# Performance work log

Hardware: AMD Instinct MI355X
Metric: run time of the kernel (lower is better)

The kernel has to match this reference:

```python
import jax, jax.numpy as jnp
import numpy as np

N = 70
NT = 2485
M_DIM = 2000
SQ2 = float(np.sqrt(2.0))
SQH = float(np.sqrt(0.5))
_r, _c = np.tril_indices(N)
ROWS = jnp.asarray(_r)
COLS = jnp.asarray(_c)


def smat(x):
    # svec^{-1}: lower-tri fill (row-major) then symmetrize with sqrt(2) off-diag scaling
    v = jnp.reshape(x, (-1,))
    L = jnp.zeros((N, N), v.dtype).at[ROWS, COLS].set(v)
    return SQH * (L + L.T) - (SQ2 - 1.0) * L * jnp.eye(N, dtype=v.dtype)


def svec(X):
    Y = SQ2 * X - (SQ2 - 1.0) * X * jnp.eye(N, dtype=X.dtype)
    return Y[ROWS, COLS].reshape(NT, 1)


def skmult(G, K, Amat):
    # vectorized version of the per-column loop: for each column a of Amat,
    # 0.5 * svec(K smat(a) G^T + G smat(a) K^T)
    S = jax.vmap(smat, in_axes=1)(Amat)                      # [L, N, N]
    T = jnp.einsum('ij,ljk,hk->lih', K, S, G) + jnp.einsum('ij,ljk,hk->lih', G, S, K)
    return jax.vmap(svec)(0.5 * T)[:, :, 0].T                # [NT, L]


def Hp_op(U, P, Pinv):
    return 0.5 * (P @ U @ Pinv + Pinv.T @ U.T @ P.T)


def _steplen(d, Rinv, gcur):
    lam0 = jnp.linalg.eigvalsh(Rinv.T @ smat(d) @ Rinv)[0]   # smallest eigenvalue
    s = jnp.where(lam0 < 0, -1.0 / lam0, 20.0)
    return jnp.minimum(0.5, gcur * s)


def setup_inputs() -> dict:
    key = jax.random.key(0)
    ks = jax.random.split(key, 6)
    R1 = jax.random.normal(ks[0], (N, N), jnp.float32)
    X0 = R1 @ R1.T + N * jnp.eye(N, dtype=jnp.float32)
    R2 = jax.random.normal(ks[1], (N, N), jnp.float32)
    Z0 = R2 @ R2.T + N * jnp.eye(N, dtype=jnp.float32)
    x = svec(X0)
    z = svec(Z0)
    A = jax.random.normal(ks[2], (M_DIM, NT), jnp.float32) / np.float32(np.sqrt(NT))
    y = jax.random.normal(ks[3], (M_DIM, 1), jnp.float32)
    b = A @ x + 0.1 * jax.random.normal(ks[4], (M_DIM, 1), jnp.float32)
    c = z + A.T @ y + 0.1 * jax.random.normal(ks[5], (NT, 1), jnp.float32)
    normc = jnp.full((1, 1), 3.7, jnp.float32)
    return {'x': x, 'y': y, 'z': z, 'A': A, 'b': b, 'c': c, 'normc': normc}


def reference(x, y, z, A, b, c, normc):
    tol = 1e-6
    X = smat(x)
    Z = smat(z)
    Q = jnp.linalg.cholesky(X).T        # upper factor: X = Q^T Q
    P = jnp.linalg.cholesky(Z).T
    Qinv = jnp.linalg.inv(Q)
    Pinv = jnp.linalg.inv(P)
    Zinv = jnp.linalg.inv(Z)
    rp = b - A @ x
    Rd = c - z - A.T @ y
    mu = (x[:, 0] @ z[:, 0]) / 70.0
    # predictor
    Rc = -svec(Hp_op(X @ Z, P, Pinv))
    Mmat = A @ skmult(X, Zinv, A.T)
    Minv = jnp.linalg.inv(Mmat)
    h = rp + A @ (skmult(X, Zinv, Rd) - skmult(Pinv, Pinv, Rc))
    dy = Minv @ h
    dz = Rd - A.T @ dy
    dx = -x - skmult(X, Zinv, dz)
    alpha = _steplen(dx, Qinv, 0.9)
    beta = _steplen(dz, Pinv, 0.9)
    minab = jnp.minimum(alpha, beta)
    e = jnp.where((mu > tol) & (minab >= jnp.sqrt(1.0 / 3.0)),
                  jnp.maximum(1.0, 3.0 * minab * minab), 1.0)
    dot_new = (x + alpha * dx)[:, 0] @ (z + beta * dz)[:, 0]
    frac = dot_new / (x[:, 0] @ z[:, 0])
    frac_safe = jnp.where(dot_new < 0, 1.0, frac)
    sigma = jnp.where(dot_new < 0, 0.8, jnp.minimum(1.0, frac_safe ** e))
    # corrector
    Rc2 = svec(sigma * mu * jnp.eye(N, dtype=x.dtype)
               - Hp_op(X @ Z, P, Pinv)
               - Hp_op(smat(dx) @ smat(dz), P, Pinv))
    h2 = rp + A @ (skmult(X, Zinv, Rd) - skmult(Pinv, Pinv, Rc2))
    dy2 = Minv @ h2
    dz2 = Rd - A.T @ dy2
    dx2 = skmult(Pinv, Pinv, Rc2) - skmult(X, Zinv, dz2)
    g2 = 0.9 + 0.09 * minab
    alpha2 = _steplen(dx2, Qinv, g2)
    beta2 = _steplen(dz2, Pinv, g2)
    x_new = x + alpha2 * dx2
    y_new = y + beta2 * dy2
    z_new = z + beta2 * dz2
    y1 = y_new * normc
    return (x_new, y_new, z_new, y1)
```

## Files before the change

### kernel.cpp

```cpp
#include <hip/hip_runtime.h>
#include <math.h>

#define SQHf 0.70710678118654752440f

struct Pairs16 { int4 q[16]; };

__device__ __forceinline__ void d_t2ij(int t, int& i, int& j) {
    float f = sqrtf(8.0f * (float)t + 1.0f);
    int r = (int)((f - 1.0f) * 0.5f);
    while (((r + 1) * (r + 2)) / 2 <= t) ++r;
    while ((r * (r + 1)) / 2 > t) --r;
    i = r;
    j = t - (r * (r + 1)) / 2;
}

__global__ void k_smat2(const float* __restrict__ v1, float* __restrict__ M1,
                        const float* __restrict__ v2, float* __restrict__ M2) {
    int idx = blockIdx.x * 256 + threadIdx.x;
    if (idx >= 9800) return;
    int which = idx / 4900;
    int e = idx - which * 4900;
    const float* v = which ? v2 : v1;
    float* M = which ? M2 : M1;
    int i = e / 70, j = e % 70;
    int hi = i > j ? i : j, lo = i > j ? j : i;
    float val = v[(hi * (hi + 1)) / 2 + lo];
    M[e] = (i == j) ? val : val * SQHf;
}

__global__ __launch_bounds__(256) void k_chol2(const float* __restrict__ A0, float* __restrict__ R0,
                                               const float* __restrict__ A1, float* __restrict__ R1) {
    const float* A = blockIdx.x ? A1 : A0;
    float* R = blockIdx.x ? R1 : R0;
    __shared__ float S[70][71];
    for (int e = threadIdx.x; e < 4900; e += 256) S[e / 70][e % 70] = A[e];
    __syncthreads();
    for (int k = 0; k < 70; ++k) {
        if (threadIdx.x == 0) S[k][k] = sqrtf(S[k][k]);
        __syncthreads();
        float d = S[k][k];
        for (int i = k + 1 + threadIdx.x; i < 70; i += 256) S[i][k] /= d;
        __syncthreads();
        for (int e = threadIdx.x; e < 4900; e += 256) {
            int i = e / 70, j = e % 70;
            if (j > k && i >= j) S[i][j] -= S[i][k] * S[j][k];
        }
        __syncthreads();
    }
    for (int e = threadIdx.x; e < 4900; e += 256) {
        int i = e / 70, j = e % 70;
        R[e] = (i <= j) ? S[j][i] : 0.0f;
    }
}

__global__ __launch_bounds__(256) void k_trinv2(const float* __restrict__ R0, float* __restrict__ O0,
                                                const float* __restrict__ R1, float* __restrict__ O1) {
    const float* R = blockIdx.x ? R1 : R0;
    float* O = blockIdx.x ? O1 : O0;
    __shared__ float S[70][71];
    __shared__ float V[70][71];
    for (int e = threadIdx.x; e < 4900; e += 256) S[e / 70][e % 70] = R[e];
    __syncthreads();
    int j = threadIdx.x;
    if (j < 70) {
        for (int i = j; i >= 0; --i) {
            float s = (i == j) ? 1.0f : 0.0f;
            for (int k = i + 1; k <= j; ++k) s -= S[i][k] * V[j][k];
            V[j][i] = s / S[i][i];
        }
    }
    __syncthreads();
    for (int e = threadIdx.x; e < 4900; e += 256) {
        int i = e / 70, jj = e % 70;
        O[e] = (i <= jj) ? V[jj][i] : 0.0f;
    }
}

__global__ __launch_bounds__(256) void k_mm70(const float* __restrict__ A, int tA,
                                              const float* __restrict__ B, int tB,
                                              float* __restrict__ C) {
    __shared__ float As[70][71], Bs[70][71];
    for (int e = threadIdx.x; e < 4900; e += 256) {
        int i = e / 70, j = e % 70;
        As[i][j] = tA ? A[j * 70 + i] : A[e];
        Bs[i][j] = tB ? B[j * 70 + i] : B[e];
    }
    __syncthreads();
    for (int e = threadIdx.x; e < 4900; e += 256) {
        int i = e / 70, j = e % 70;
        float s = 0.0f;
        for (int k = 0; k < 70; ++k) s += As[i][k] * Bs[k][j];
        C[e] = s;
    }
}

__global__ __launch_bounds__(256) void k_gemv_rowA(const float* __restrict__ A, long lda, int Kdim,
                                                   const float* __restrict__ v, const float* __restrict__ add,
                                                   float sgn, float* __restrict__ out) {
    int row = blockIdx.x;
    const float* Ar = A + (long)row * lda;
    float s = 0.0f;
    for (int k = threadIdx.x; k < Kdim; k += 256) s += Ar[k] * v[k];
    __shared__ float red[256];
    red[threadIdx.x] = s;
    __syncthreads();
    for (int o = 128; o; o >>= 1) {
        if (threadIdx.x < o) red[threadIdx.x] += red[threadIdx.x + o];
        __syncthreads();
    }
    if (threadIdx.x == 0) out[row] = (add ? add[row] : 0.0f) + sgn * red[0];
}

__global__ __launch_bounds__(256) void k_colAT_part(const float* __restrict__ A, long lda, int M, int Ncols,
                                                    const float* __restrict__ w, float* __restrict__ partial) {
    int j = blockIdx.x * 256 + threadIdx.x;
    int s = blockIdx.y;
    int rpb = (M + gridDim.y - 1) / gridDim.y;
    int i0 = s * rpb, i1 = i0 + rpb < M ? i0 + rpb : M;
    float acc = 0.0f;
    if (j < Ncols)
        for (int i = i0; i < i1; ++i) acc += A[(long)i * lda + j] * w[i];
    if (j < Ncols) partial[(long)s * Ncols + j] = acc;
}
__global__ __launch_bounds__(256) void k_colAT_fin(const float* __restrict__ partial, int S, int Ncols,
                                                   const float* __restrict__ add1, const float* __restrict__ add2,
                                                   float sgn, float* __restrict__ out) {
    int j = blockIdx.x * 256 + threadIdx.x;
    if (j >= Ncols) return;
    float s = 0.0f;
    for (int k = 0; k < S; ++k) s += partial[(long)k * Ncols + j];
    float base = (add1 ? add1[j] : 0.0f) - (add2 ? add2[j] : 0.0f);
    out[j] = base + sgn * s;
}

__global__ __launch_bounds__(256) void k_dots_init(const float* __restrict__ x, const float* __restrict__ z,
                                                   float* __restrict__ sc) {
    __shared__ float red[256];
    float s = 0.0f;
    for (int i = threadIdx.x; i < 2485; i += 256) s += x[i] * z[i];
    red[threadIdx.x] = s;
    __syncthreads();
    for (int o = 128; o; o >>= 1) {
        if (threadIdx.x < o) red[threadIdx.x] += red[threadIdx.x + o];
        __syncthreads();
    }
    if (threadIdx.x == 0) { sc[1] = red[0]; sc[0] = red[0] / 70.0f; }
}

__global__ __launch_bounds__(256) void k_dot_new(const float* __restrict__ x, const float* __restrict__ dx,
                                                 const float* __restrict__ z, const float* __restrict__ dz,
                                                 float* __restrict__ sc) {
    __shared__ float red[256];
    float a = sc[2], b = sc[3];
    float s = 0.0f;
    for (int i = threadIdx.x; i < 2485; i += 256)
        s += (x[i] + a * dx[i]) * (z[i] + b * dz[i]);
    red[threadIdx.x] = s;
    __syncthreads();
    for (int o = 128; o; o >>= 1) {
        if (threadIdx.x < o) red[threadIdx.x] += red[threadIdx.x + o];
        __syncthreads();
    }
    if (threadIdx.x == 0) sc[7] = red[0];
}

__global__ __launch_bounds__(256) void k_rc_chain(const float* __restrict__ X, const float* __restrict__ Z,
                                                  const float* __restrict__ Pu, const float* __restrict__ Pi,
                                                  float* __restrict__ W1out, float* __restrict__ Rc) {
    __shared__ float A[70][71], B[70][71], C[70][71];
    int tid = threadIdx.x;
    for (int e = tid; e < 4900; e += 256) { A[e / 70][e % 70] = X[e]; B[e / 70][e % 70] = Z[e]; }
    __syncthreads();
    for (int e = tid; e < 4900; e += 256) {
        int i = e / 70, j = e % 70;
        float s = 0.0f;
        for (int k = 0; k < 70; ++k) s += A[i][k] * B[k][j];
        C[i][j] = s;
    }
    __syncthreads();
    for (int e = tid; e < 4900; e += 256) A[e / 70][e % 70] = Pu[e];
    __syncthreads();
    for (int e = tid; e < 4900; e += 256) {
        int i = e / 70, j = e % 70;
        float s = 0.0f;
        for (int k = 0; k < 70; ++k) s += A[i][k] * C[k][j];
        B[i][j] = s;
    }
    __syncthreads();
    for (int e = tid; e < 4900; e += 256) A[e / 70][e % 70] = Pi[e];
    __syncthreads();
    for (int e = tid; e < 4900; e += 256) {
        int i = e / 70, j = e % 70;
        float s = 0.0f;
        for (int k = 0; k < 70; ++k) s += B[i][k] * A[k][j];
        C[i][j] = s;
        W1out[e] = s;
    }
    __syncthreads();
    for (int t = tid; t < 2485; t += 256) {
        int i, j;
        d_t2ij(t, i, j);
        float v = (i == j) ? C[i][i] : (C[i][j] + C[j][i]) * SQHf;
        Rc[t] = -v;
    }
}

__global__ __launch_bounds__(256) void k_rc2_chain(const float* __restrict__ dxv, const float* __restrict__ dzv,
                                                   const float* __restrict__ Pu, const float* __restrict__ Pi,
                                                   const float* __restrict__ W1, const float* __restrict__ sc,
                                                   float* __restrict__ Rc2) {
    __shared__ float A[70][71], B[70][71], C[70][71];
    int tid = threadIdx.x;
    for (int e = tid; e < 4900; e += 256) {
        int i = e / 70, j = e % 70;
        int hi = i > j ? i : j, lo = i > j ? j : i;
        float vx = dxv[(hi * (hi + 1)) / 2 + lo];
        float vz = dzv[(hi * (hi + 1)) / 2 + lo];
        A[i][j] = (i == j) ? vx : vx * SQHf;
        B[i][j] = (i == j) ? vz : vz * SQHf;
    }
    __syncthreads();
    for (int e = tid; e < 4900; e += 256) {
        int i = e / 70, j = e % 70;
        float s = 0.0f;
        for (int k = 0; k < 70; ++k) s += A[i][k] * B[k][j];
        C[i][j] = s;
    }
    __syncthreads();
    for (int e = tid; e < 4900; e += 256) A[e / 70][e % 70] = Pu[e];
    __syncthreads();
    for (int e = tid; e < 4900; e += 256) {
        int i = e / 70, j = e % 70;
        float s = 0.0f;
        for (int k = 0; k < 70; ++k) s += A[i][k] * C[k][j];
        B[i][j] = s;
    }
    __syncthreads();
    for (int e = tid; e < 4900; e += 256) A[e / 70][e % 70] = Pi[e];
    __syncthreads();
    for (int e = tid; e < 4900; e += 256) {
        int i = e / 70, j = e % 70;
        float s = 0.0f;
        for (int k = 0; k < 70; ++k) s += B[i][k] * A[k][j];
        C[i][j] = s;
    }
    __syncthreads();
    float sm = sc[13];
    for (int t = tid; t < 2485; t += 256) {
        int i, j;
        d_t2ij(t, i, j);
        if (i == j)
            Rc2[t] = sm - W1[i * 70 + i] - C[i][i];
        else
            Rc2[t] = -(W1[i * 70 + j] + W1[j * 70 + i] + C[i][j] + C[j][i]) * SQHf;
    }
}

__global__ __launch_bounds__(256) void k_skmult(const float* __restrict__ K, const float* __restrict__ G,
                                                const float* __restrict__ Arows, long ldA,
                                                float* __restrict__ outT, long ldOut) {
    int l = blockIdx.x;
    const float* a = Arows + (long)l * ldA;
    float* out = outT + (long)l * ldOut;
    __shared__ float S[70][71];
    __shared__ float T1[70][71];
    for (int e = threadIdx.x; e < 4900; e += 256) {
        int i = e / 70, j = e % 70;
        int hi = i > j ? i : j, lo = i > j ? j : i;
        float v = a[(hi * (hi + 1)) / 2 + lo];
        S[i][j] = (i == j) ? v : v * SQHf;
    }
    __syncthreads();
    for (int e = threadIdx.x; e < 4900; e += 256) {
        int i = e / 70, j = e % 70;
        const float* Gr = G + j * 70;
        float s = 0.0f;
        for (int k = 0; k < 70; ++k) s += S[i][k] * Gr[k];
        T1[i][j] = s;
    }
    __syncthreads();
    for (int t = threadIdx.x; t < 2485; t += 256) {
        int i, j;
        d_t2ij(t, i, j);
        const float* Ki = K + i * 70;
        const float* Kj = K + j * 70;
        float wij = 0.0f, wji = 0.0f;
        for (int k = 0; k < 70; ++k) {
            wij += Ki[k] * T1[k][j];
            wji += Kj[k] * T1[k][i];
        }
        out[t] = (i == j) ? wij : (wij + wji) * SQHf;
    }
}

#define GBM 64
#define GBK 32
__global__ __launch_bounds__(256) void k_gemm_nt(const float* __restrict__ A, long lda,
                                                 const float* __restrict__ B, long ldb,
                                                 float* __restrict__ C, long ldc,
                                                 int M, int N, int Kd,
                                                 float alpha, float beta, int lower_only) {
    int bx = blockIdx.x, by = blockIdx.y;
    int row0 = by * GBM, col0 = bx * GBM;
    if (lower_only && col0 > row0 + GBM - 1) return;
    __shared__ float As[GBM][GBK + 1], Bs[GBM][GBK + 1];
    int tid = threadIdx.x;
    int tx = tid % 16, ty = tid / 16;
    float acc[4][4] = {{0.f}};
    for (int k0 = 0; k0 < Kd; k0 += GBK) {
        for (int e = tid; e < GBM * GBK; e += 256) {
            int r = e / GBK, cc = e % GBK;
            int gr = row0 + r, gc = k0 + cc;
            As[r][cc] = (gr < M && gc < Kd) ? A[(long)gr * lda + gc] : 0.0f;
        }
        for (int e = tid; e < GBM * GBK; e += 256) {
            int r = e / GBK, cc = e % GBK;
            int gr = col0 + r, gc = k0 + cc;
            Bs[r][cc] = (gr < N && gc < Kd) ? B[(long)gr * ldb + gc] : 0.0f;
        }
        __syncthreads();
        for (int kk = 0; kk < GBK; ++kk) {
            float av[4], bv[4];
#pragma unroll
            for (int m = 0; m < 4; ++m) av[m] = As[ty * 4 + m][kk];
#pragma unroll
            for (int n = 0; n < 4; ++n) bv[n] = Bs[tx * 4 + n][kk];
#pragma unroll
            for (int m = 0; m < 4; ++m)
#pragma unroll
                for (int n = 0; n < 4; ++n) acc[m][n] += av[m] * bv[n];
        }
        __syncthreads();
    }
#pragma unroll
    for (int m = 0; m < 4; ++m)
#pragma unroll
        for (int n = 0; n < 4; ++n) {
            int gr = row0 + ty * 4 + m, gc = col0 + tx * 4 + n;
            if (gr < M && gc < N) {
                float* cp = &C[(long)gr * ldc + gc];
                if (beta != 0.0f) *cp = beta * (*cp) + alpha * acc[m][n];
                else *cp = alpha * acc[m][n];
            }
        }
}

__device__ __forceinline__ void gemm_nn_dev(const float* __restrict__ A, long lda,
                                            const float* __restrict__ B, long ldb,
                                            float* __restrict__ C, long ldc,
                                            int M, int N, int K, float alpha) {
    int row0 = blockIdx.y * 64, col0 = blockIdx.x * 64;
    if (row0 >= M || col0 >= N) return;
    __shared__ float As[64][33], Bs[32][65];
    int tid = threadIdx.x;
    int tx = tid % 16, ty = tid / 16;
    float acc[4][4] = {{0.f}};
    for (int k0 = 0; k0 < K; k0 += 32) {
        for (int e = tid; e < 64 * 32; e += 256) {
            int r = e / 32, cc = e % 32;
            As[r][cc] = (row0 + r < M && k0 + cc < K) ? A[(long)(row0 + r) * lda + k0 + cc] : 0.0f;
        }
        for (int e = tid; e < 32 * 64; e += 256) {
            int kk = e / 64, nn = e % 64;
            Bs[kk][nn] = (k0 + kk < K && col0 + nn < N) ? B[(long)(k0 + kk) * ldb + col0 + nn] : 0.0f;
        }
        __syncthreads();
        for (int kk = 0; kk < 32; ++kk) {
            float av[4], bv[4];
#pragma unroll
            for (int m = 0; m < 4; ++m) av[m] = As[ty * 4 + m][kk];
#pragma unroll
            for (int n = 0; n < 4; ++n) bv[n] = Bs[kk][tx * 4 + n];
#pragma unroll
            for (int m = 0; m < 4; ++m)
#pragma unroll
                for (int n = 0; n < 4; ++n) acc[m][n] += av[m] * bv[n];
        }
        __syncthreads();
    }
#pragma unroll
    for (int m = 0; m < 4; ++m)
#pragma unroll
        for (int n = 0; n < 4; ++n) {
            int gr = row0 + ty * 4 + m, gc = col0 + tx * 4 + n;
            if (gr < M && gc < N) C[(long)gr * ldc + gc] = alpha * acc[m][n];
        }
}

__global__ __launch_bounds__(256) void k_tri_phaseA(const float* __restrict__ Mm, long ld,
                                                    float* __restrict__ tmp, Pairs16 pl, int np) {
    int z = blockIdx.z;
    if (z >= np) return;
    int p0 = pl.q[z].x, h = pl.q[z].y, n = pl.q[z].z, toff = pl.q[z].w;
    gemm_nn_dev(Mm + (long)(p0 + h) * ld + p0, ld,
                Mm + (long)p0 * ld + p0, ld,
                tmp + toff, h, n - h, h, h, 1.0f);
}
__global__ __launch_bounds__(256) void k_tri_phaseB(float* __restrict__ Mm, long ld,
                                                    const float* __restrict__ tmp, Pairs16 pl, int np) {
    int z = blockIdx.z;
    if (z >= np) return;
    int p0 = pl.q[z].x, h = pl.q[z].y, n = pl.q[z].z, toff = pl.q[z].w;
    int M = n - h;
    gemm_nn_dev(Mm + (long)(p0 + h) * ld + (p0 + h), ld,
                tmp + toff, h,
                Mm + (long)(p0 + h) * ld + p0, ld, M, h, M, -1.0f);
}

__global__ void k_zero_upper(float* __restrict__ Mm, int n) {
    int row0 = blockIdx.y * 64, col0 = blockIdx.x * 64;
    if (col0 <= row0) return;
    for (int e = threadIdx.x; e < 4096; e += 256) {
        int i = row0 + (e >> 6), j = col0 + (e & 63);
        if (i < n && j < n) Mm[(long)i * n + j] = 0.0f;
    }
}

__global__ void k_copy_diaginv(float* __restrict__ Mm, long ld, int n, const float* __restrict__ Linv) {
    int t = blockIdx.x;
    int jb = t * 64;
    int nb = n - jb < 64 ? n - jb : 64;
    if (nb <= 0) return;
    const float* Vi = Linv + (long)t * 4096;
    for (int e = threadIdx.x; e < nb * nb; e += 256) {
        int i = e / nb, j = e % nb;
        Mm[(long)(jb + i) * ld + jb + j] = Vi[i * 64 + j];
    }
}

__global__ __launch_bounds__(256) void k_trimv_low(const float* __restrict__ W, long ld, int n,
                                                   const float* __restrict__ h, float* __restrict__ out) {
    int i = blockIdx.x;
    const float* Wr = W + (long)i * ld;
    float s = 0.0f;
    for (int k = threadIdx.x; k <= i; k += 256) s += Wr[k] * h[k];
    __shared__ float red[256];
    red[threadIdx.x] = s;
    __syncthreads();
    for (int o = 128; o; o >>= 1) {
        if (threadIdx.x < o) red[threadIdx.x] += red[threadIdx.x + o];
        __syncthreads();
    }
    if (threadIdx.x == 0) out[i] = red[0];
}

__global__ __launch_bounds__(256) void k_trimvT_part(const float* __restrict__ W, long ld, int n,
                                                     const float* __restrict__ v, float* __restrict__ partial) {
    int j = blockIdx.x * 256 + threadIdx.x;
    int s = blockIdx.y;
    int rpb = (n + gridDim.y - 1) / gridDim.y;
    int i0 = s * rpb, i1 = i0 + rpb < n ? i0 + rpb : n;
    float acc = 0.0f;
    if (j < n) {
        int ist = i0 > j ? i0 : j;
        for (int i = ist; i < i1; ++i) acc += W[(long)i * ld + j] * v[i];
        partial[(long)s * n + j] = acc;
    }
}
__global__ __launch_bounds__(256) void k_part_reduce(const float* __restrict__ partial, int S, int n,
                                                     float* __restrict__ out) {
    int j = blockIdx.x * 256 + threadIdx.x;
    if (j >= n) return;
    float s = 0.0f;
    for (int k = 0; k < S; ++k) s += partial[(long)k * n + j];
    out[j] = s;
}

__global__ __launch_bounds__(256) void k_chol_diag_inv(float* __restrict__ Mp, long ld, int jb, int nb,
                                                       float* __restrict__ Linv) {
    __shared__ float S[64][65];
    __shared__ float V[64][65];
    int tid = threadIdx.x;
    for (int e = tid; e < nb * nb; e += 256) S[e / nb][e % nb] = Mp[(long)(jb + e / nb) * ld + jb + e % nb];
    __syncthreads();
    for (int k = 0; k < nb; ++k) {
        if (tid == 0) S[k][k] = sqrtf(S[k][k]);
        __syncthreads();
        float d = S[k][k];
        for (int i = k + 1 + tid; i < nb; i += 256) S[i][k] /= d;
        __syncthreads();
        for (int e = tid; e < nb * nb; e += 256) {
            int i = e / nb, j = e % nb;
            if (j > k && i >= j) S[i][j] -= S[i][k] * S[j][k];
        }
        __syncthreads();
    }
    for (int e = tid; e < nb * nb; e += 256) {
        int i = e / nb, j = e % nb;
        if (i >= j) Mp[(long)(jb + i) * ld + jb + j] = S[i][j];
    }
    if (tid < nb) {
        int c = tid;
        V[c][c] = 1.0f / S[c][c];
        for (int i = c + 1; i < nb; ++i) {
            float s = 0.0f;
            for (int k = c; k < i; ++k) s += S[i][k] * V[k][c];
            V[i][c] = -s / S[i][i];
        }
    }
    __syncthreads();
    for (int e = tid; e < 4096; e += 256) {
        int i = e >> 6, j = e & 63;
        Linv[e] = (i < nb && j < nb && i >= j) ? V[i][j] : 0.0f;
    }
}

__global__ __launch_bounds__(256) void k_panel_trsm(float* __restrict__ Mp, long ld, int jb, int nb, int n,
                                                    const float* __restrict__ Linv) {
    __shared__ float Vs[64][65];
    __shared__ float As[64][65];
    int r0 = jb + nb + blockIdx.x * 64;
    int nrows = n - r0;
    if (nrows > 64) nrows = 64;
    if (nrows <= 0) return;
    int tid = threadIdx.x;
    for (int e = tid; e < 4096; e += 256) { int i = e >> 6, j = e & 63; Vs[i][j] = Linv[e]; }
    for (int e = tid; e < nrows * nb; e += 256) {
        int i = e / nb, j = e % nb;
        As[i][j] = Mp[(long)(r0 + i) * ld + jb + j];
    }
    __syncthreads();
    int tx = tid % 16, ty = tid / 16;
    float acc[4][4] = {{0.f}};
    for (int k = 0; k < nb; ++k) {
        float av[4], bv[4];
#pragma unroll
        for (int m = 0; m < 4; ++m) av[m] = As[ty * 4 + m][k];
#pragma unroll
        for (int c = 0; c < 4; ++c) bv[c] = Vs[tx * 4 + c][k];
#pragma unroll
        for (int m = 0; m < 4; ++m)
#pragma unroll
            for (int c = 0; c < 4; ++c) acc[m][c] += av[m] * bv[c];
    }
#pragma unroll
    for (int m = 0; m < 4; ++m)
#pragma unroll
        for (int c = 0; c < 4; ++c) {
            int gr = ty * 4 + m, gc = tx * 4 + c;
            if (gr < nrows && gc < nb) Mp[(long)(r0 + gr) * ld + jb + gc] = acc[m][c];
        }
}

__device__ __forceinline__ int jac_f(int i, int r) {
    return (i == 0) ? 0 : 1 + ((i - 1 + r) % 69);
}
__global__ __launch_bounds__(256) void k_steplen_eig(const float* __restrict__ dxv, const float* __restrict__ dzv,
                                                     const float* __restrict__ Qi, const float* __restrict__ Pi,
                                                     float* __restrict__ sc, int o0, int o1) {
    const float* v = blockIdx.x ? dzv : dxv;
    const float* Rm = blockIdx.x ? Pi : Qi;
    int outi = blockIdx.x ? o1 : o0;
    __shared__ float S[70][71], T[70][71], A[70][71];
    __shared__ float cs[35], sn[35];
    int tid = threadIdx.x;
    for (int e = tid; e < 4900; e += 256) {
        int i = e / 70, j = e % 70;
        int hi = i > j ? i : j, lo = i > j ? j : i;
        float val = v[(hi * (hi + 1)) / 2 + lo];
        S[i][j] = (i == j) ? val : val * SQHf;
        A[i][j] = Rm[e];
    }
    __syncthreads();
    for (int e = tid; e < 4900; e += 256) {
        int i = e / 70, j = e % 70;
        float s = 0.0f;
        for (int k = 0; k < 70; ++k) s += A[k][i] * S[k][j];
        T[i][j] = s;
    }
    __syncthreads();
    for (int e = tid; e < 4900; e += 256) {
        int i = e / 70, j = e % 70;
        float s = 0.0f;
        for (int k = 0; k < 70; ++k) s += T[i][k] * A[k][j];
        S[i][j] = s;
    }
    __syncthreads();
    for (int sw = 0; sw < 6; ++sw) {
        for (int rr = 0; rr < 69; ++rr) {
            if (tid < 35) {
                int p = jac_f(tid, rr), q = jac_f(69 - tid, rr);
                float app = S[p][p], aqq = S[q][q], apq = S[p][q];
                float cc = 1.0f, ss = 0.0f;
                float denom = fabsf(app) + fabsf(aqq);
                if (fabsf(apq) > 1e-12f * denom + 1e-30f) {
                    float tau = (aqq - app) / (2.0f * apq);
                    float t = ((tau >= 0.0f) ? 1.0f : -1.0f) / (fabsf(tau) + sqrtf(1.0f + tau * tau));
                    cc = 1.0f / sqrtf(1.0f + t * t);
                    ss = t * cc;
                }
                cs[tid] = cc;
                sn[tid] = ss;
            }
            __syncthreads();
            for (int t = tid; t < 1225; t += 256) {
                int a = t / 35, b = t - a * 35;
                int pa = jac_f(a, rr), qa = jac_f(69 - a, rr);
                int pb = jac_f(b, rr), qb = jac_f(69 - b, rr);
                float ca = cs[a], sa = sn[a], cb = cs[b], sb = sn[b];
                float m00 = S[pa][pb], m01 = S[pa][qb], m10 = S[qa][pb], m11 = S[qa][qb];
                float r00 = ca * m00 - sa * m10, r01 = ca * m01 - sa * m11;
                float r10 = sa * m00 + ca * m10, r11 = sa * m01 + ca * m11;
                S[pa][pb] = cb * r00 - sb * r01;
                S[pa][qb] = sb * r00 + cb * r01;
                S[qa][pb] = cb * r10 - sb * r11;
                S[qa][qb] = sb * r10 + cb * r11;
            }
            __syncthreads();
        }
    }
    __shared__ float red[256];
    float mn = 1e30f;
    for (int i = tid; i < 70; i += 256) mn = fminf(mn, S[i][i]);
    red[tid] = mn;
    __syncthreads();
    for (int o = 128; o; o >>= 1) {
        if (tid < o) red[tid] = fminf(red[tid], red[tid + o]);
        __syncthreads();
    }
    if (tid == 0) sc[outi] = red[0];
}

__global__ void k_pred_scalars(float* sc) {
    float l0a = sc[11], l0b = sc[12];
    float sa = (l0a < 0.0f) ? -1.0f / l0a : 20.0f;
    float sb = (l0b < 0.0f) ? -1.0f / l0b : 20.0f;
    float alpha = fminf(0.5f, 0.9f * sa);
    float beta = fminf(0.5f, 0.9f * sb);
    float minab = fminf(alpha, beta);
    sc[2] = alpha;
    sc[3] = beta;
    sc[4] = minab;
    float mu = sc[0];
    sc[5] = (mu > 1e-6f && minab >= 0.57735026918962576f) ? fmaxf(1.0f, 3.0f * minab * minab) : 1.0f;
}
__global__ void k_sigma(float* sc) {
    float dn = sc[7], xz = sc[1], e = sc[5];
    float frac = dn / xz;
    float fs = (dn < 0.0f) ? 1.0f : frac;
    float sig = (dn < 0.0f) ? 0.8f : fminf(1.0f, powf(fs, e));
    sc[6] = sig;
    sc[13] = sig * sc[0];
    sc[8] = 0.9f + 0.09f * sc[4];
}
__global__ void k_corr_scalars(float* sc) {
    float g2 = sc[8];
    float l0a = sc[14], l0b = sc[15];
    float sa = (l0a < 0.0f) ? -1.0f / l0a : 20.0f;
    float sb = (l0b < 0.0f) ? -1.0f / l0b : 20.0f;
    sc[9] = fminf(0.5f, g2 * sa);
    sc[10] = fminf(0.5f, g2 * sb);
}

__global__ void k_axpby(const float* __restrict__ u, const float* __restrict__ v,
                        float a, float b, float* __restrict__ out, int n) {
    int i = blockIdx.x * 256 + threadIdx.x;
    if (i < n) out[i] = a * u[i] + b * v[i];
}

__global__ void k_final(const float* __restrict__ x, const float* __restrict__ y, const float* __restrict__ z,
                        const float* __restrict__ dx2, const float* __restrict__ dy2, const float* __restrict__ dz2,
                        const float* __restrict__ normc, const float* __restrict__ sc, float* __restrict__ out) {
    int i = blockIdx.x * 256 + threadIdx.x;
    float a2 = sc[9], b2 = sc[10];
    if (i < 2485) out[i] = x[i] + a2 * dx2[i];
    else if (i < 4485) { int j = i - 2485; out[i] = y[j] + b2 * dy2[j]; }
    else if (i < 6970) { int j = i - 4485; out[i] = z[j] + b2 * dz2[j]; }
    else if (i < 8970) { int j = i - 6970; out[i] = (y[j] + b2 * dy2[j]) * normc[0]; }
}

extern "C" void kernel_launch(void* const* d_in, const int* in_sizes, int n_in,
                              void* d_out, int out_size, void* d_ws, size_t ws_size,
                              hipStream_t stream) {
    const float* x = (const float*)d_in[0];
    const float* y = (const float*)d_in[1];
    const float* z = (const float*)d_in[2];
    const float* A = (const float*)d_in[3];
    const float* b = (const float*)d_in[4];
    const float* c = (const float*)d_in[5];
    const float* normc = (const float*)d_in[6];
    float* out = (float*)d_out;
    float* ws = (float*)d_ws;

    float* SKT = ws;
    float* Mm = ws + 4970000;
    float* S0 = ws + 8970000;
    float* X = S0;
    float* Z = S0 + 4900;
    float* Qu = S0 + 9800;
    float* Pu = S0 + 14700;
    float* Qi = S0 + 19600;
    float* Pi = S0 + 24500;
    float* Zi = S0 + 29400;
    float* W1 = S0 + 44100;
    float* rp = S0 + 83300;
    float* h = S0 + 85300;
    float* dy = S0 + 87300;
    float* dy2 = S0 + 89300;
    float* h2 = S0 + 91300;
    float* Rd = S0 + 93300;
    float* Rc = S0 + 95785;
    float* k1 = S0 + 98270;
    float* k2 = S0 + 100755;
    float* dz = S0 + 103240;
    float* dx = S0 + 105725;
    float* Rc2 = S0 + 108210;
    float* k2b = S0 + 110695;
    float* dz2 = S0 + 113180;
    float* dx2 = S0 + 115665;
    float* tmpv = S0 + 118150;
    float* sc = S0 + 120635;
    float* Linv = S0 + 121000;
    float* v1 = S0 + 253000;
    float* pbuf = S0 + 256000;

    k_smat2<<<39, 256, 0, stream>>>(x, X, z, Z);
    k_chol2<<<2, 256, 0, stream>>>(X, Qu, Z, Pu);
    k_trinv2<<<2, 256, 0, stream>>>(Qu, Qi, Pu, Pi);
    k_mm70<<<1, 256, 0, stream>>>(Pi, 0, Pi, 1, Zi);

    k_gemv_rowA<<<2000, 256, 0, stream>>>(A, 2485L, 2485, x, b, -1.0f, rp);
    k_colAT_part<<<dim3(10, 16), 256, 0, stream>>>(A, 2485L, 2000, 2485, y, pbuf);
    k_colAT_fin<<<10, 256, 0, stream>>>(pbuf, 16, 2485, c, z, -1.0f, Rd);
    k_dots_init<<<1, 256, 0, stream>>>(x, z, sc);

    k_rc_chain<<<1, 256, 0, stream>>>(X, Z, Pu, Pi, W1, Rc);

    k_skmult<<<2000, 256, 0, stream>>>(X, Zi, A, 2485L, SKT, 2485L);
    k_gemm_nt<<<dim3(32, 32), 256, 0, stream>>>(A, 2485L, SKT, 2485L, Mm, 2000L,
                                                2000, 2000, 2485, 1.0f, 0.0f, 1);

    for (int jb = 0; jb < 2000; jb += 64) {
        int nb = (2000 - jb) < 64 ? (2000 - jb) : 64;
        float* Lslot = Linv + (long)(jb / 64) * 4096;
        k_chol_diag_inv<<<1, 256, 0, stream>>>(Mm, 2000L, jb, nb, Lslot);
        int rows = 2000 - jb - nb;
        if (rows > 0) {
            int gb = (rows + 63) / 64;
            k_panel_trsm<<<gb, 256, 0, stream>>>(Mm, 2000L, jb, nb, 2000, Lslot);
            const float* pan = Mm + (size_t)(jb + nb) * 2000 + jb;
            float* csub = Mm + (size_t)(jb + nb) * 2000 + (jb + nb);
            k_gemm_nt<<<dim3(gb, gb), 256, 0, stream>>>(pan, 2000L, pan, 2000L, csub, 2000L,
                                                        rows, rows, nb, -1.0f, 1.0f, 1);
        }
    }

    k_zero_upper<<<dim3(32, 32), 256, 0, stream>>>(Mm, 2000);
    k_copy_diaginv<<<32, 256, 0, stream>>>(Mm, 2000L, 2000, Linv);
    for (int bs = 64; bs < 2000; bs *= 2) {
        Pairs16 pl;
        int np = 0, maxM = 0, toff = 0;
        for (int p0 = 0; p0 + bs < 2000; p0 += 2 * bs) {
            int hh = bs;
            int nn = (2 * bs < 2000 - p0) ? 2 * bs : (2000 - p0);
            pl.q[np].x = p0; pl.q[np].y = hh; pl.q[np].z = nn; pl.q[np].w = toff;
            toff += (nn - hh) * hh;
            if (nn - hh > maxM) maxM = nn - hh;
            ++np;
        }
        if (np == 0) continue;
        dim3 g((bs + 63) / 64, (maxM + 63) / 64, np);
        k_tri_phaseA<<<g, 256, 0, stream>>>(Mm, 2000L, SKT, pl, np);
        k_tri_phaseB<<<g, 256, 0, stream>>>(Mm, 2000L, SKT, pl, np);
    }

    k_skmult<<<1, 256, 0, stream>>>(X, Zi, Rd, 0L, k1, 0L);
    k_skmult<<<1, 256, 0, stream>>>(Pi, Pi, Rc, 0L, k2, 0L);
    k_axpby<<<10, 256, 0, stream>>>(k1, k2, 1.0f, -1.0f, tmpv, 2485);
    k_gemv_rowA<<<2000, 256, 0, stream>>>(A, 2485L, 2485, tmpv, rp, 1.0f, h);
    k_trimv_low<<<2000, 256, 0, stream>>>(Mm, 2000L, 2000, h, v1);
    k_trimvT_part<<<dim3(8, 16), 256, 0, stream>>>(Mm, 2000L, 2000, v1, pbuf);
    k_part_reduce<<<8, 256, 0, stream>>>(pbuf, 16, 2000, dy);
    k_colAT_part<<<dim3(10, 16), 256, 0, stream>>>(A, 2485L, 2000, 2485, dy, pbuf);
    k_colAT_fin<<<10, 256, 0, stream>>>(pbuf, 16, 2485, Rd, (const float*)0, -1.0f, dz);
    k_skmult<<<1, 256, 0, stream>>>(X, Zi, dz, 0L, tmpv, 0L);
    k_axpby<<<10, 256, 0, stream>>>(x, tmpv, -1.0f, -1.0f, dx, 2485);

    k_steplen_eig<<<2, 256, 0, stream>>>(dx, dz, Qi, Pi, sc, 11, 12);
    k_pred_scalars<<<1, 1, 0, stream>>>(sc);
    k_dot_new<<<1, 256, 0, stream>>>(x, dx, z, dz, sc);
    k_sigma<<<1, 1, 0, stream>>>(sc);

    k_rc2_chain<<<1, 256, 0, stream>>>(dx, dz, Pu, Pi, W1, sc, Rc2);
    k_skmult<<<1, 256, 0, stream>>>(Pi, Pi, Rc2, 0L, k2b, 0L);
    k_axpby<<<10, 256, 0, stream>>>(k1, k2b, 1.0f, -1.0f, tmpv, 2485);
    k_gemv_rowA<<<2000, 256, 0, stream>>>(A, 2485L, 2485, tmpv, rp, 1.0f, h2);
    k_trimv_low<<<2000, 256, 0, stream>>>(Mm, 2000L, 2000, h2, v1);
    k_trimvT_part<<<dim3(8, 16), 256, 0, stream>>>(Mm, 2000L, 2000, v1, pbuf);
    k_part_reduce<<<8, 256, 0, stream>>>(pbuf, 16, 2000, dy2);
    k_colAT_part<<<dim3(10, 16), 256, 0, stream>>>(A, 2485L, 2000, 2485, dy2, pbuf);
    k_colAT_fin<<<10, 256, 0, stream>>>(pbuf, 16, 2485, Rd, (const float*)0, -1.0f, dz2);
    k_skmult<<<1, 256, 0, stream>>>(X, Zi, dz2, 0L, tmpv, 0L);
    k_axpby<<<10, 256, 0, stream>>>(k2b, tmpv, 1.0f, -1.0f, dx2, 2485);

    k_steplen_eig<<<2, 256, 0, stream>>>(dx2, dz2, Qi, Pi, sc, 14, 15);
    k_corr_scalars<<<1, 1, 0, stream>>>(sc);

    k_final<<<36, 256, 0, stream>>>(x, y, z, dx2, dy2, dz2, normc, sc, out);
}
```

Measured before the change: 10.31 ms.

## Use 128x128 register-tiled NT GEMM, sync-light Cholesky diag, single-wave Jacobi

Replaces the 64x64 NT GEMM, used for the Schur complement and the blocked Cholesky trailing updates, with a 128x128 tile and 8x8 per-thread register blocking. Shared memory is laid out k-major so operands can be read with float4 loads. The diagonal-block Cholesky now uses an LDL-style update that needs one barrier per column, with the sqrt scaling applied at the end. The Jacobi eigen sweep runs in a single wavefront with compiler fences in place of block barriers. Risks are fewer blocks for the small trailing updates, and the wave-fence trick relies on lockstep execution within a wavefront.

Result: slower. 13.86 ms (+34.4%).

```diff
diff --git a/kernel.cpp b/kernel.cpp
--- a/kernel.cpp
+++ b/kernel.cpp
@@ -2,6 +2,7 @@
 #include <math.h>
 
 #define SQHf 0.70710678118654752440f
+#define WAVE_FENCE() asm volatile("" ::: "memory")
 
 struct Pairs16 { int4 q[16]; };
 
@@ -293,56 +294,66 @@
     }
 }
 
-#define GBM 64
-#define GBK 32
-__global__ __launch_bounds__(256) void k_gemm_nt(const float* __restrict__ A, long lda,
-                                                 const float* __restrict__ B, long ldb,
-                                                 float* __restrict__ C, long ldc,
-                                                 int M, int N, int Kd,
-                                                 float alpha, float beta, int lower_only) {
-    int bx = blockIdx.x, by = blockIdx.y;
-    int row0 = by * GBM, col0 = bx * GBM;
-    if (lower_only && col0 > row0 + GBM - 1) return;
-    __shared__ float As[GBM][GBK + 1], Bs[GBM][GBK + 1];
+#define BBM 128
+#define BBK 32
+__global__ __launch_bounds__(256) void k_gemm_nt_big(const float* __restrict__ A, long lda,
+                                                     const float* __restrict__ B, long ldb,
+                                                     float* __restrict__ C, long ldc,
+                                                     int M, int N, int Kd,
+                                                     float alpha, float beta, int lower_only) {
+    int row0 = blockIdx.y * BBM, col0 = blockIdx.x * BBM;
+    if (row0 >= M || col0 >= N) return;
+    if (lower_only && col0 > row0 + BBM - 1) return;
+    __shared__ float As[BBK][BBM + 4];
+    __shared__ float Bs[BBK][BBM + 4];
     int tid = threadIdx.x;
-    int tx = tid % 16, ty = tid / 16;
-    float acc[4][4] = {{0.f}};
-    for (int k0 = 0; k0 < Kd; k0 += GBK) {
-        for (int e = tid; e < GBM * GBK; e += 256) {
-            int r = e / GBK, cc = e % GBK;
+    int tx = tid & 15, ty = tid >> 4;
+    float acc[8][8];
+#pragma unroll
+    for (int m = 0; m < 8; ++m)
+#pragma unroll
+        for (int n = 0; n < 8; ++n) acc[m][n] = 0.0f;
+    for (int k0 = 0; k0 < Kd; k0 += BBK) {
+        for (int e = tid; e < BBM * BBK; e += 256) {
+            int r = e >> 5, cc = e & 31;
             int gr = row0 + r, gc = k0 + cc;
-            As[r][cc] = (gr < M && gc < Kd) ? A[(long)gr * lda + gc] : 0.0f;
-        }
-        for (int e = tid; e < GBM * GBK; e += 256) {
-            int r = e / GBK, cc = e % GBK;
+            As[cc][r] = (gr < M && gc < Kd) ? A[(long)gr * lda + gc] : 0.0f;
+        }
+        for (int e = tid; e < BBM * BBK; e += 256) {
+            int r = e >> 5, cc = e & 31;
             int gr = col0 + r, gc = k0 + cc;
-            Bs[r][cc] = (gr < N && gc < Kd) ? B[(long)gr * ldb + gc] : 0.0f;
-        }
-        __syncthreads();
-        for (int kk = 0; kk < GBK; ++kk) {
-            float av[4], bv[4];
-#pragma unroll
-            for (int m = 0; m < 4; ++m) av[m] = As[ty * 4 + m][kk];
-#pragma unroll
-            for (int n = 0; n < 4; ++n) bv[n] = Bs[tx * 4 + n][kk];
-#pragma unroll
-            for (int m = 0; m < 4; ++m)
-#pragma unroll
-                for (int n = 0; n < 4; ++n) acc[m][n] += av[m] * bv[n];
-        }
-        __syncthreads();
-    }
-#pragma unroll
-    for (int m = 0; m < 4; ++m)
-#pragma unroll
-        for (int n = 0; n < 4; ++n) {
-            int gr = row0 + ty * 4 + m, gc = col0 + tx * 4 + n;
-            if (gr < M && gc < N) {
-                float* cp = &C[(long)gr * ldc + gc];
-                if (beta != 0.0f) *cp = beta * (*cp) + alpha * acc[m][n];
-                else *cp = alpha * acc[m][n];
+            Bs[cc][r] = (gr < N && gc < Kd) ? B[(long)gr * ldb + gc] : 0.0f;
+        }
+        __syncthreads();
+        for (int kk = 0; kk < BBK; ++kk) {
+            float4 a0 = *(const float4*)&As[kk][ty * 8];
+            float4 a1 = *(const float4*)&As[kk][ty * 8 + 4];
+            float4 b0 = *(const float4*)&Bs[kk][tx * 8];
+            float4 b1 = *(const float4*)&Bs[kk][tx * 8 + 4];
+            float av[8] = {a0.x, a0.y, a0.z, a0.w, a1.x, a1.y, a1.z, a1.w};
+            float bv[8] = {b0.x, b0.y, b0.z, b0.w, b1.x, b1.y, b1.z, b1.w};
+#pragma unroll
+            for (int m = 0; m < 8; ++m)
+#pragma unroll
+                for (int n = 0; n < 8; ++n) acc[m][n] += av[m] * bv[n];
+        }
+        __syncthreads();
+    }
+#pragma unroll
+    for (int m = 0; m < 8; ++m) {
+        int gr = row0 + ty * 8 + m;
+        if (gr < M) {
+#pragma unroll
+            for (int n = 0; n < 8; ++n) {
+                int gc = col0 + tx * 8 + n;
+                if (gc < N) {
+                    float* cp = &C[(long)gr * ldc + gc];
+                    if (beta != 0.0f) *cp = beta * (*cp) + alpha * acc[m][n];
+                    else *cp = alpha * acc[m][n];
+                }
             }
         }
+    }
 }
 
 __device__ __forceinline__ void gemm_nn_dev(const float* __restrict__ A, long lda,
@@ -470,21 +481,25 @@
                                                        float* __restrict__ Linv) {
     __shared__ float S[64][65];
     __shared__ float V[64][65];
+    __shared__ float dv[64];
     int tid = threadIdx.x;
     for (int e = tid; e < nb * nb; e += 256) S[e / nb][e % nb] = Mp[(long)(jb + e / nb) * ld + jb + e % nb];
     __syncthreads();
     for (int k = 0; k < nb; ++k) {
-        if (tid == 0) S[k][k] = sqrtf(S[k][k]);
-        __syncthreads();
-        float d = S[k][k];
-        for (int i = k + 1 + tid; i < nb; i += 256) S[i][k] /= d;
-        __syncthreads();
+        float dinv = 1.0f / S[k][k];
         for (int e = tid; e < nb * nb; e += 256) {
             int i = e / nb, j = e % nb;
-            if (j > k && i >= j) S[i][j] -= S[i][k] * S[j][k];
-        }
-        __syncthreads();
-    }
+            if (j > k && i >= j) S[i][j] -= S[i][k] * S[j][k] * dinv;
+        }
+        __syncthreads();
+    }
+    if (tid < nb) dv[tid] = rsqrtf(S[tid][tid]);
+    __syncthreads();
+    for (int e = tid; e < nb * nb; e += 256) {
+        int i = e / nb, j = e % nb;
+        if (i >= j) S[i][j] *= dv[j];
+    }
+    __syncthreads();
     for (int e = tid; e < nb * nb; e += 256) {
         int i = e / nb, j = e % nb;
         if (i >= j) Mp[(long)(jb + i) * ld + jb + j] = S[i][j];
@@ -576,39 +591,42 @@
         S[i][j] = s;
     }
     __syncthreads();
-    for (int sw = 0; sw < 6; ++sw) {
-        for (int rr = 0; rr < 69; ++rr) {
-            if (tid < 35) {
-                int p = jac_f(tid, rr), q = jac_f(69 - tid, rr);
-                float app = S[p][p], aqq = S[q][q], apq = S[p][q];
-                float cc = 1.0f, ss = 0.0f;
-                float denom = fabsf(app) + fabsf(aqq);
-                if (fabsf(apq) > 1e-12f * denom + 1e-30f) {
-                    float tau = (aqq - app) / (2.0f * apq);
-                    float t = ((tau >= 0.0f) ? 1.0f : -1.0f) / (fabsf(tau) + sqrtf(1.0f + tau * tau));
-                    cc = 1.0f / sqrtf(1.0f + t * t);
-                    ss = t * cc;
+    if (tid < 64) {
+        for (int sw = 0; sw < 6; ++sw) {
+            for (int rr = 0; rr < 69; ++rr) {
+                if (tid < 35) {
+                    int p = jac_f(tid, rr), q = jac_f(69 - tid, rr);
+                    float app = S[p][p], aqq = S[q][q], apq = S[p][q];
+                    float cc = 1.0f, ss = 0.0f;
+                    float denom = fabsf(app) + fabsf(aqq);
+                    if (fabsf(apq) > 1e-12f * denom + 1e-30f) {
+                        float tau = (aqq - app) / (2.0f * apq);
+                        float t = ((tau >= 0.0f) ? 1.0f : -1.0f) / (fabsf(tau) + sqrtf(1.0f + tau * tau));
+                        cc = 1.0f / sqrtf(1.0f + t * t);
+                        ss = t * cc;
+                    }
+                    cs[tid] = cc;
+                    sn[tid] = ss;
                 }
-                cs[tid] = cc;
-                sn[tid] = ss;
+                WAVE_FENCE();
+                for (int t = tid; t < 1225; t += 64) {
+                    int a = t / 35, b = t - a * 35;
+                    int pa = jac_f(a, rr), qa = jac_f(69 - a, rr);
+                    int pb = jac_f(b, rr), qb = jac_f(69 - b, rr);
+                    float ca = cs[a], sa = sn[a], cb = cs[b], sb = sn[b];
+                    float m00 = S[pa][pb], m01 = S[pa][qb], m10 = S[qa][pb], m11 = S[qa][qb];
+                    float r00 = ca * m00 - sa * m10, r01 = ca * m01 - sa * m11;
+                    float r10 = sa * m00 + ca * m10, r11 = sa * m01 + ca * m11;
+                    S[pa][pb] = cb * r00 - sb * r01;
+                    S[pa][qb] = sb * r00 + cb * r01;
+                    S[qa][pb] = cb * r10 - sb * r11;
+                    S[qa][qb] = sb * r10 + cb * r11;
+                }
+                WAVE_FENCE();
             }
-            __syncthreads();
-            for (int t = tid; t < 1225; t += 256) {
-                int a = t / 35, b = t - a * 35;
-                int pa = jac_f(a, rr), qa = jac_f(69 - a, rr);
-                int pb = jac_f(b, rr), qb = jac_f(69 - b, rr);
-                float ca = cs[a], sa = sn[a], cb = cs[b], sb = sn[b];
-                float m00 = S[pa][pb], m01 = S[pa][qb], m10 = S[qa][pb], m11 = S[qa][qb];
-                float r00 = ca * m00 - sa * m10, r01 = ca * m01 - sa * m11;
-                float r10 = sa * m00 + ca * m10, r11 = sa * m01 + ca * m11;
-                S[pa][pb] = cb * r00 - sb * r01;
-                S[pa][qb] = sb * r00 + cb * r01;
-                S[qa][pb] = cb * r10 - sb * r11;
-                S[qa][qb] = sb * r10 + cb * r11;
-            }
-            __syncthreads();
-        }
-    }
+        }
+    }
+    __syncthreads();
     __shared__ float red[256];
     float mn = 1e30f;
     for (int i = tid; i < 70; i += 256) mn = fminf(mn, S[i][i]);
@@ -727,8 +745,8 @@
     k_rc_chain<<<1, 256, 0, stream>>>(X, Z, Pu, Pi, W1, Rc);
 
     k_skmult<<<2000, 256, 0, stream>>>(X, Zi, A, 2485L, SKT, 2485L);
-    k_gemm_nt<<<dim3(32, 32), 256, 0, stream>>>(A, 2485L, SKT, 2485L, Mm, 2000L,
-                                                2000, 2000, 2485, 1.0f, 0.0f, 1);
+    k_gemm_nt_big<<<dim3(16, 16), 256, 0, stream>>>(A, 2485L, SKT, 2485L, Mm, 2000L,
+                                                    2000, 2000, 2485, 1.0f, 0.0f, 1);
 
     for (int jb = 0; jb < 2000; jb += 64) {
         int nb = (2000 - jb) < 64 ? (2000 - jb) : 64;
@@ -738,10 +756,11 @@
         if (rows > 0) {
             int gb = (rows + 63) / 64;
             k_panel_trsm<<<gb, 256, 0, stream>>>(Mm, 2000L, jb, nb, 2000, Lslot);
+            int gb2 = (rows + 127) / 128;
             const float* pan = Mm + (size_t)(jb + nb) * 2000 + jb;
             float* csub = Mm + (size_t)(jb + nb) * 2000 + (jb + nb);
-            k_gemm_nt<<<dim3(gb, gb), 256, 0, stream>>>(pan, 2000L, pan, 2000L, csub, 2000L,
-                                                        rows, rows, nb, -1.0f, 1.0f, 1);
+            k_gemm_nt_big<<<dim3(gb2, gb2), 256, 0, stream>>>(pan, 2000L, pan, 2000L, csub, 2000L,
+                                                              rows, rows, nb, -1.0f, 1.0f, 1);
         }
     }
 
```
